# Kernel optimization log

Hardware: AMD Instinct MI355X
Metric: run time of the kernel (lower is better)

The kernel has to match this reference:

```python
import jax, jax.numpy as jnp
import numpy as np
from jax.scipy.optimize import minimize

LAMDA = 0.01        # lamda default in MI()
N_DOMAINS = 2       # domain_label is binary (source/target)
MAXITER = 50        # BFGS iteration budget (torchmin l-bfgs analogue)


def _sq_dists(A, B):
    # squared euclidean pairwise distances == torch.cdist(A, B, p=2) ** 2
    an = jnp.sum(A * A, axis=-1)
    bn = jnp.sum(B * B, axis=-1)
    return an[:, None] + bn[None, :] - 2.0 * (A @ B.T)


def _median_sigma(sf):
    # sigma = median of nonzero squared pairwise source distances.
    # With continuous features the only zeros are the diagonal, so mask it.
    pd = jnp.maximum(_sq_dists(sf, sf), 0.0)
    pd = jnp.where(jnp.eye(pd.shape[0], dtype=bool), jnp.nan, pd)
    return jnp.nanmedian(pd)


def _build(sf, tf, y, l):
    # Gaussian kernel masked by class agreement, plus domain one-hots.
    sigma = _median_sigma(sf)
    X = jnp.concatenate([sf, tf], axis=0)              # [N, d]
    D = _sq_dists(X, X)                                 # [N, N]
    Deltay = (y[:, None] == y[None, :]).astype(X.dtype)
    K_W = jnp.exp(-D / sigma) * Deltay                  # [N, N]
    onehot = jax.nn.one_hot(l[:, 0], N_DOMAINS, dtype=X.dtype)  # [N, 2]
    KD = K_W * (onehot @ onehot.T)                      # K_W * Deltal
    w = jnp.sum(onehot, axis=0) / X.shape[0]            # domain counts / N
    return K_W, KD, onehot, w


def _div(theta, K_W, KD, onehot, w):
    # mean((K_W*Deltal) @ theta) - mean(exp((theta*K_W) @ Deltal - 1))
    # Deltal = onehot @ onehot.T (rank-2), so the second NxN @ NxN matmul
    # collapses to A = K_W @ (theta[:,None]*onehot) with column weights w.
    term1 = jnp.mean(KD @ theta)
    A = K_W @ (theta[:, None] * onehot)                 # [N, 2]
    term2 = jnp.mean(jnp.exp(A - 1.0) @ w)
    return term1 - term2


def _solve_theta(K_W, KD, onehot, w):
    N = K_W.shape[0]
    obj = lambda th: -_div(th, K_W, KD, onehot, w) + LAMDA * (th @ th)
    res = minimize(obj, jnp.zeros((N,), K_W.dtype), method="BFGS",
                   options={"maxiter": MAXITER})
    return res.x


def setup_inputs() -> dict:
    key = jax.random.key(0)
    k1, k2, k3, k4 = jax.random.split(key, 4)
    B, d, n_class = 2048, 256, 31
    source_features = jax.random.normal(k1, (B, d), dtype=jnp.float32)
    target_features = jax.random.normal(k2, (B, d), dtype=jnp.float32)
    y = jax.random.randint(k3, (2 * B,), 0, n_class, dtype=jnp.int32)
    l = jax.random.randint(k4, (2 * B, 1), 0, N_DOMAINS, dtype=jnp.int32)
    return {"source_features": source_features, "target_features": target_features,
            "y": y, "l": l}


def reference(source_features, target_features, y, l):
    K_W, KD, onehot, w = _build(source_features, target_features, y, l)
    theta_hat = _solve_theta(K_W, KD, onehot, w)
    return _div(theta_hat, K_W, KD, onehot, w)
```

## Files before the change

kernel.cpp:

```cpp
#include <hip/hip_runtime.h>
#include <math.h>

#define N_TOT   4096
#define N_SRC   2048
#define DIMF    256
#define NCLASS  31
#define LAMBDA  0.01f

#define K_TRI1  1048063LL
#define K_TRI2  1048064LL

#define WS_ACC    0
#define WS_HIST0  64
#define WS_HISTA  16448
#define WS_HISTB  32832
#define WS_H2A    49216
#define WS_H2B    50240
#define WS_STATE  51264
#define WS_TICK   51520
#define WS_META   52288
#define WS_SCAL   52800
#define ZERO_BYTES 53248
#define WS_PERM   53248
#define WS_XN     69632
#define WS_DS     1048576
#define WS_KBLK   17825792

#define MAXW 224
#define MAXM 112
#define WPAD 116

__device__ __forceinline__ float bf2f(unsigned short h) {
  return __uint_as_float(((unsigned)h) << 16);
}

__device__ __forceinline__ float wredF(float v) {
#pragma unroll
  for (int o = 1; o < 64; o <<= 1) v += __shfl_xor(v, o, 64);
  return v;
}

__device__ __forceinline__ double blockReduceSum(double v, double* red) {
#pragma unroll
  for (int o = 32; o > 0; o >>= 1) v += __shfl_down(v, o, 64);
  int w = threadIdx.x >> 6, lane = threadIdx.x & 63;
  __syncthreads();
  if (lane == 0) red[w] = v;
  __syncthreads();
  return red[0] + red[1] + red[2] + red[3];
}

__device__ __forceinline__ void blockReduceSumMax(double s, double mx, double* red,
                                                  double& os, double& om) {
#pragma unroll
  for (int o = 32; o > 0; o >>= 1) {
    s += __shfl_down(s, o, 64);
    double u = __shfl_down(mx, o, 64);
    mx = fmax(mx, u);
  }
  int w = threadIdx.x >> 6, lane = threadIdx.x & 63;
  __syncthreads();
  if (lane == 0) { red[w] = s; red[4 + w] = mx; }
  __syncthreads();
  os = red[0] + red[1] + red[2] + red[3];
  om = fmax(fmax(red[4], red[5]), fmax(red[6], red[7]));
}

__device__ void scan_find(const unsigned* hist, int nbins, long long k, unsigned* shOut) {
  __shared__ long long tsum[256];
  int tid = threadIdx.x;
  int per = nbins / 256;
  long long s = 0;
  for (int q = 0; q < per; q++) s += hist[tid * per + q];
  tsum[tid] = s;
  __syncthreads();
  long long acc = s;
  for (int off = 1; off < 256; off <<= 1) {
    long long add = (tid >= off) ? tsum[tid - off] : 0;
    __syncthreads();
    acc += add;
    tsum[tid] = acc;
    __syncthreads();
  }
  long long run = acc - s;
  for (int q = 0; q < per; q++) {
    unsigned c = hist[tid * per + q];
    if (k >= run && k < run + (long long)c) { shOut[0] = (unsigned)(tid * per + q); shOut[1] = (unsigned)(k - run); }
    run += c;
  }
  __syncthreads();
}

__global__ __launch_bounds__(256) void xn_kernel(const float* __restrict__ sf,
                                                 const float* __restrict__ tf,
                                                 float* __restrict__ xn) {
  int wid = threadIdx.x >> 6, lane = threadIdx.x & 63;
  int row = blockIdx.x * 4 + wid;
  const float* src = (row < N_SRC) ? (sf + (size_t)row * DIMF) : (tf + (size_t)(row - N_SRC) * DIMF);
  float4 v = ((const float4*)src)[lane];
  float s = v.x * v.x + v.y * v.y + v.z * v.z + v.w * v.w;
#pragma unroll
  for (int o = 32; o > 0; o >>= 1) s += __shfl_down(s, o, 64);
  if (lane == 0) xn[row] = s;
}

__global__ __launch_bounds__(256) void dist_k(const float* __restrict__ sf,
                                              const float* __restrict__ xn,
                                              float* __restrict__ Ds,
                                              unsigned* __restrict__ h) {
  __shared__ float As[16][68];
  __shared__ float Bs[16][68];
  __shared__ unsigned lh[4096];
  const int tx = threadIdx.x, ty = threadIdx.y;
  const int tid = ty * 16 + tx;
  for (int q = tid; q < 4096; q += 256) lh[q] = 0;
  int b = blockIdx.x;
  int by = (int)((sqrtf(8.f * (float)b + 1.f) - 1.f) * 0.5f);
  while ((by + 1) * (by + 2) / 2 <= b) ++by;
  while (by * (by + 1) / 2 > b) --by;
  int bx = b - by * (by + 1) / 2;
  const int R = by * 64, C = bx * 64;
  const int si = tid >> 2, sq = tid & 3;
  float4 va = ((const float4*)(sf + (size_t)(R + si) * 256 + 0))[sq];
  float4 vb = ((const float4*)(sf + (size_t)(C + si) * 256 + 0))[sq];
  float acc[4][4] = {};
  for (int kc = 0; kc < 256; kc += 16) {
    As[sq * 4 + 0][si] = va.x; As[sq * 4 + 1][si] = va.y; As[sq * 4 + 2][si] = va.z; As[sq * 4 + 3][si] = va.w;
    Bs[sq * 4 + 0][si] = vb.x; Bs[sq * 4 + 1][si] = vb.y; Bs[sq * 4 + 2][si] = vb.z; Bs[sq * 4 + 3][si] = vb.w;
    __syncthreads();
    if (kc + 16 < 256) {
      va = ((const float4*)(sf + (size_t)(R + si) * 256 + kc + 16))[sq];
      vb = ((const float4*)(sf + (size_t)(C + si) * 256 + kc + 16))[sq];
    }
#pragma unroll
    for (int k = 0; k < 16; k++) {
      float4 a = *(const float4*)&As[k][ty * 4];
      float4 b2 = *(const float4*)&Bs[k][tx * 4];
      acc[0][0] += a.x * b2.x; acc[0][1] += a.x * b2.y; acc[0][2] += a.x * b2.z; acc[0][3] += a.x * b2.w;
      acc[1][0] += a.y * b2.x; acc[1][1] += a.y * b2.y; acc[1][2] += a.y * b2.z; acc[1][3] += a.y * b2.w;
      acc[2][0] += a.z * b2.x; acc[2][1] += a.z * b2.y; acc[2][2] += a.z * b2.z; acc[2][3] += a.z * b2.w;
      acc[3][0] += a.w * b2.x; acc[3][1] += a.w * b2.y; acc[3][2] += a.w * b2.z; acc[3][3] += a.w * b2.w;
    }
    __syncthreads();
  }
  int jbase = C + tx * 4;
  float xnj0 = xn[jbase + 0], xnj1 = xn[jbase + 1], xnj2 = xn[jbase + 2], xnj3 = xn[jbase + 3];
#pragma unroll
  for (int r = 0; r < 4; r++) {
    int i = R + ty * 4 + r;
    float xni = xn[i];
    float v[4];
    v[0] = fmaxf(xni + xnj0 - 2.f * acc[r][0], 0.f);
    v[1] = fmaxf(xni + xnj1 - 2.f * acc[r][1], 0.f);
    v[2] = fmaxf(xni + xnj2 - 2.f * acc[r][2], 0.f);
    v[3] = fmaxf(xni + xnj3 - 2.f * acc[r][3], 0.f);
    if (jbase + 3 < i) {
      float4 o; o.x = v[0]; o.y = v[1]; o.z = v[2]; o.w = v[3];
      ((float4*)&Ds[(size_t)i * 2048 + jbase])[0] = o;
      atomicAdd(&lh[__float_as_uint(v[0]) >> 20], 1u);
      atomicAdd(&lh[__float_as_uint(v[1]) >> 20], 1u);
      atomicAdd(&lh[__float_as_uint(v[2]) >> 20], 1u);
      atomicAdd(&lh[__float_as_uint(v[3]) >> 20], 1u);
    } else {
#pragma unroll
      for (int k = 0; k < 4; k++) {
        if (jbase + k < i) {
          Ds[(size_t)i * 2048 + jbase + k] = v[k];
          atomicAdd(&lh[__float_as_uint(v[k]) >> 20], 1u);
        }
      }
    }
  }
  __syncthreads();
  for (int q = tid; q < 4096; q += 256) if (lh[q]) atomicAdd(&h[q], lh[q]);
}

__global__ __launch_bounds__(256) void scan0_k(const unsigned* __restrict__ h, unsigned* __restrict__ st) {
  __shared__ unsigned r0[2];
  __shared__ unsigned r1[2];
  scan_find(h, 4096, K_TRI1, r0);
  scan_find(h, 4096, K_TRI2, r1);
  if (threadIdx.x == 0) { st[0] = r0[0]; st[1] = r0[1]; st[2] = r1[0]; st[3] = r1[1]; }
}

__global__ __launch_bounds__(256) void hist1_k(const float* __restrict__ Ds, const unsigned* __restrict__ st,
                                               unsigned* __restrict__ hA, unsigned* __restrict__ hB) {
  __shared__ unsigned lA[4096];
  __shared__ unsigned lB[4096];
  for (int i = threadIdx.x; i < 4096; i += 256) { lA[i] = 0; lB[i] = 0; }
  __syncthreads();
  unsigned s0 = st[0], s1 = st[2];
  int gw = (blockIdx.x * 256 + threadIdx.x) >> 6;
  int lane = threadIdx.x & 63;
  const float* row = Ds + (size_t)gw * 2048;
  for (int j = lane; j < gw; j += 64) {
    unsigned u = __float_as_uint(row[j]);
    unsigned hi = u >> 20, mid = (u >> 8) & 0xFFFu;
    if (hi == s0) atomicAdd(&lA[mid], 1u);
    if (hi == s1) atomicAdd(&lB[mid], 1u);
  }
  __syncthreads();
  for (int i = threadIdx.x; i < 4096; i += 256) {
    if (lA[i]) atomicAdd(&hA[i], lA[i]);
    if (lB[i]) atomicAdd(&hB[i], lB[i]);
  }
}

__global__ __launch_bounds__(256) void scan1_k(const unsigned* __restrict__ hA, const unsigned* __restrict__ hB,
                                               unsigned* __restrict__ st) {
  __shared__ unsigned r0[2];
  __shared__ unsigned r1[2];
  long long kA = (long long)st[1];
  long long kB = (long long)st[3];
  scan_find(hA, 4096, kA, r0);
  scan_find(hB, 4096, kB, r1);
  if (threadIdx.x == 0) { st[4] = r0[0]; st[5] = r0[1]; st[6] = r1[0]; st[7] = r1[1]; }
}

__global__ __launch_bounds__(256) void hist2_k(const float* __restrict__ Ds, const unsigned* __restrict__ st,
                                               unsigned* __restrict__ hA, unsigned* __restrict__ hB) {
  __shared__ unsigned lA[256];
  __shared__ unsigned lB[256];
  lA[threadIdx.x] = 0; lB[threadIdx.x] = 0;
  __syncthreads();
  unsigned p0 = (st[0] << 12) | st[4];
  unsigned p1 = (st[2] << 12) | st[6];
  int gw = (blockIdx.x * 256 + threadIdx.x) >> 6;
  int lane = threadIdx.x & 63;
  const float* row = Ds + (size_t)gw * 2048;
  for (int j = lane; j < gw; j += 64) {
    unsigned u = __float_as_uint(row[j]);
    unsigned pre = u >> 8;
    if (pre == p0) atomicAdd(&lA[u & 0xFFu], 1u);
    if (pre == p1) atomicAdd(&lB[u & 0xFFu], 1u);
  }
  __syncthreads();
  if (lA[threadIdx.x]) atomicAdd(&hA[threadIdx.x], lA[threadIdx.x]);
  if (lB[threadIdx.x]) atomicAdd(&hB[threadIdx.x], lB[threadIdx.x]);
}

__global__ __launch_bounds__(256) void scan2b_k(const unsigned* __restrict__ hA, const unsigned* __restrict__ hB,
                                                const unsigned* __restrict__ st, float* __restrict__ scal,
                                                const int* __restrict__ y, const int* __restrict__ l,
                                                int* __restrict__ perm, int* __restrict__ meta) {
  int tid = threadIdx.x;
  __shared__ unsigned r0[2];
  __shared__ unsigned r1[2];
  scan_find(hA, 256, (long long)st[5], r0);
  scan_find(hB, 256, (long long)st[7], r1);
  if (tid == 0) {
    unsigned v1 = (st[0] << 20) | (st[4] << 8) | r0[0];
    unsigned v2 = (st[2] << 20) | (st[6] << 8) | r1[0];
    scal[0] = 0.5f * (__uint_as_float(v1) + __uint_as_float(v2));
  }
  __shared__ unsigned cl[64];
  __shared__ unsigned bs2[64];
  __shared__ unsigned cur[64];
  if (tid < 64) cl[tid] = 0;
  __syncthreads();
  for (int i = tid; i < N_TOT; i += 256) atomicAdd(&cl[y[i] * 2 + l[i]], 1u);
  __syncthreads();
  if (tid == 0) {
    unsigned run = 0;
    for (int b2 = 0; b2 < 62; b2++) { bs2[b2] = run; run += cl[b2]; }
    unsigned run2 = 0, cnt0 = 0;
    for (int c = 0; c < NCLASS; c++) {
      int n = (int)(cl[2 * c] + cl[2 * c + 1]);
      meta[c] = n; meta[32 + c] = (int)cl[2 * c]; meta[64 + c] = (int)bs2[2 * c];
      meta[96 + c] = (int)run2; run2 += (unsigned)(n * n);
      cnt0 += cl[2 * c];
    }
    scal[1] = (float)((double)cnt0 / (4096.0 * 4096.0));
    scal[2] = (float)((double)(N_TOT - cnt0) / (4096.0 * 4096.0));
  }
  __syncthreads();
  if (tid < 64) cur[tid] = bs2[tid];
  __syncthreads();
  for (int i = tid; i < N_TOT; i += 256) {
    int b2 = y[i] * 2 + l[i];
    unsigned pos = atomicAdd(&cur[b2], 1u);
    perm[pos] = i;
  }
}

__global__ __launch_bounds__(256) void build_k(const float* __restrict__ sf, const float* __restrict__ tf,
                                               const float* __restrict__ xn, const int* __restrict__ perm,
                                               const int* __restrict__ meta, const float* __restrict__ scal,
                                               float* __restrict__ gK) {
  const int c = blockIdx.z;
  const int n = meta[c];
  const int cs = meta[64 + c];
  const int bo = meta[96 + c];
  const int T = (n + 15) >> 4;
  int b = blockIdx.x;
  if (b >= T * (T + 1) / 2) return;
  int by = (int)((sqrtf(8.f * (float)b + 1.f) - 1.f) * 0.5f);
  while ((by + 1) * (by + 2) / 2 <= b) ++by;
  while (by * (by + 1) / 2 > b) --by;
  int bx = b - by * (by + 1) / 2;
  const int i0 = by * 16, j0 = bx * 16;
  const int tx = threadIdx.x, ty = threadIdx.y;
  __shared__ float As[16][260];
  __shared__ float Bs[16][260];
  __shared__ float ot[16][17];
  __shared__ int ra[16];
  __shared__ int rb[16];
  int tid = ty * 16 + tx;
  if (tid < 16) { int il = i0 + tid; ra[tid] = (il < n) ? perm[cs + il] : -1; }
  else if (tid < 32) { int jl = j0 + tid - 16; rb[tid - 16] = (jl < n) ? perm[cs + jl] : -1; }
  __syncthreads();
  for (int e = tid; e < 1024; e += 256) {
    int r = e >> 6, q = e & 63;
    int g = ra[r];
    if (g >= 0) {
      const float* src = (g < N_SRC) ? (sf + (size_t)g * DIMF) : (tf + (size_t)(g - N_SRC) * DIMF);
      ((float4*)&As[r][q * 4])[0] = ((const float4*)src)[q];
    }
    int g2 = rb[r];
    if (g2 >= 0) {
      const float* src = (g2 < N_SRC) ? (sf + (size_t)g2 * DIMF) : (tf + (size_t)(g2 - N_SRC) * DIMF);
      ((float4*)&Bs[r][q * 4])[0] = ((const float4*)src)[q];
    }
  }
  __syncthreads();
  int il = i0 + ty, jl = j0 + tx;
  float val = 0.f;
  if (il < n && jl < n) {
    float dot = 0.f;
    const float4* a4 = (const float4*)&As[ty][0];
    const float4* b4 = (const float4*)&Bs[tx][0];
#pragma unroll 16
    for (int q = 0; q < 64; q++) {
      float4 a = a4[q], b2 = b4[q];
      dot += a.x * b2.x + a.y * b2.y + a.z * b2.z + a.w * b2.w;
    }
    int gi = ra[ty], gj = rb[tx];
    float d = xn[gi] + xn[gj] - 2.f * dot;
    val = expf(-d / scal[0]);
    gK[(size_t)bo + (size_t)il * n + jl] = val;
  }
  ot[ty][tx] = val;
  __syncthreads();
  if (by != bx) {
    int il2 = j0 + ty, jl2 = i0 + tx;
    if (il2 < n && jl2 < n) gK[(size_t)bo + (size_t)il2 * n + jl2] = ot[tx][ty];
  }
}

__global__ __launch_bounds__(256) void solver_k(const float* __restrict__ gK, const int* __restrict__ meta,
                                                const float* __restrict__ scal, double* __restrict__ acc,
                                                unsigned* __restrict__ tick, float* __restrict__ out) {
  const int c = blockIdx.x >> 1, d = blockIdx.x & 1;
  const int n = meta[c];
  const int m0 = meta[32 + c];
  const int m = d ? (n - m0) : m0;
  const int c0 = d ? m0 : 0;
  const int bo = meta[96 + c];
  const float gamma = scal[1 + d];
  const int tid = threadIdx.x;
  const int wv = tid >> 6, lane = tid & 63;

  __shared__ unsigned short Wl[MAXW * WPAD];
  __shared__ float pS[4 * MAXM];
  __shared__ float pD[4 * MAXM];
  __shared__ float Av[MAXW];
  __shared__ float Sv[MAXW];
  __shared__ float Uv[MAXW];
  __shared__ float Bq[MAXW];
  __shared__ float bc[MAXM];
  __shared__ float gv[MAXM];
  __shared__ float dgv[MAXM];
  __shared__ alignas(16) float th[128];
  __shared__ alignas(16) float pv[128];
  __shared__ alignas(16) float xv[128];
  __shared__ double red[16];
  __shared__ double gds[2];
  __shared__ int cgst[2];

  const float* K = gK + bo;
  const int st = n;
  const int mp2 = (m + 1) & ~1;
  const int mp4 = (m + 3) & ~3;
  const int iw0 = (n * wv) >> 2, iw1 = (n * (wv + 1)) >> 2;

  for (int i = tid >> 2; i < n; i += 64) {
    const float* Kr = K + (size_t)i * st + c0;
    unsigned short* Wr = Wl + i * WPAD;
    for (int j = (tid & 3); j < m; j += 4) {
      unsigned u = __float_as_uint(Kr[j]);
      u += 0x7fffu + ((u >> 16) & 1u);
      Wr[j] = (unsigned short)(u >> 16);
    }
    if ((tid & 3) == 0) for (int j = m; j < mp4; j++) Wr[j] = 0;
  }
  {
    const int r0 = (m * wv) >> 2, r1 = (m * (wv + 1)) >> 2;
    for (int j = lane; j < m; j += 64) {
      const float* Kr = K + (size_t)(c0 + j) * st + c0;
      float s = 0.f;
      for (int r = r0; r < r1; r++) s += Kr[r];
      pS[wv * MAXM + j] = s;
    }
  }
  __syncthreads();
  for (int j = tid; j < 128; j += 256) { th[j] = 0.f; pv[j] = 0.f; xv[j] = 0.f; }
  for (int j = tid; j < m; j += 256)
    bc[j] = (pS[j] + pS[MAXM + j] + pS[2 * MAXM + j] + pS[3 * MAXM + j]) * (1.0f / 4096.0f);
  __syncthreads();

  for (int it = 0; it < 25; it++) {
    double o = 0.0;
    if (it == 0) {
      const float s0c = gamma * expf(-1.f);
      for (int i = tid; i < n; i += 256) { Av[i] = 0.f; Sv[i] = s0c; o += (double)s0c; }
    } else {
      for (int i = tid; i < n; i += 256) {
        const unsigned short* Wr = Wl + i * WPAD;
        float a = 0.f;
#pragma unroll 4
        for (int j = 0; j < mp4; j += 4) {
          unsigned long long u = *(const unsigned long long*)(Wr + j);
          float4 t4 = *(const float4*)(th + j);
          unsigned lo = (unsigned)u, hi = (unsigned)(u >> 32);
          a += __uint_as_float(lo << 16) * t4.x
             + __uint_as_float(lo & 0xffff0000u) * t4.y
             + __uint_as_float(hi << 16) * t4.z
             + __uint_as_float(hi & 0xffff0000u) * t4.w;
        }
        Av[i] = a;
        float si = gamma * expf(fminf(a - 1.f, 30.f));
        Sv[i] = si; o += (double)si;
      }
      for (int j = tid; j < m; j += 256) {
        float t_ = th[j];
        o += (double)(-bc[j] * t_ + LAMBDA * t_ * t_);
      }
    }
    __syncthreads();
    if (it == 0) {
      for (int j = lane; j < m; j += 64) {
        const unsigned short* Wc = Wl + j;
        float s_ = 0.f, ds_ = 0.f;
        int i = iw0;
        for (; i + 3 < iw1; i += 4) {
          float w0 = bf2f(Wc[(i + 0) * WPAD]), w1 = bf2f(Wc[(i + 1) * WPAD]);
          float w2 = bf2f(Wc[(i + 2) * WPAD]), w3 = bf2f(Wc[(i + 3) * WPAD]);
          float a0 = w0 * Sv[i], a1 = w1 * Sv[i + 1], a2 = w2 * Sv[i + 2], a3 = w3 * Sv[i + 3];
          s_ += a0 + a1 + a2 + a3;
          ds_ += a0 * w0 + a1 * w1 + a2 * w2 + a3 * w3;
        }
        for (; i < iw1; i++) { float w = bf2f(Wc[i * WPAD]); float a = w * Sv[i]; s_ += a; ds_ += a * w; }
        pS[wv * MAXM + j] = s_; pD[wv * MAXM + j] = ds_;
      }
    } else {
      for (int j = lane; j < m; j += 64) {
        const unsigned short* Wc = Wl + j;
        float s_ = 0.f;
        int i = iw0;
        for (; i + 3 < iw1; i += 4)
          s_ += bf2f(Wc[(i+0)*WPAD]) * Sv[i]   + bf2f(Wc[(i+1)*WPAD]) * Sv[i+1]
              + bf2f(Wc[(i+2)*WPAD]) * Sv[i+2] + bf2f(Wc[(i+3)*WPAD]) * Sv[i+3];
        for (; i < iw1; i++) s_ += bf2f(Wc[i * WPAD]) * Sv[i];
        pS[wv * MAXM + j] = s_;
      }
    }
    __syncthreads();
    double gm = 0.0;
    for (int j = tid; j < m; j += 256) {
      float s_ = pS[j] + pS[MAXM + j] + pS[2 * MAXM + j] + pS[3 * MAXM + j];
      if (it == 0) {
        float ds_ = pD[j] + pD[MAXM + j] + pD[2 * MAXM + j] + pD[3 * MAXM + j];
        dgv[j] = ds_ + 2.f * LAMBDA;
      }
      float g = s_ - bc[j] + 2.f * LAMBDA * th[j];
      gv[j] = g;
      double ag = fabs((double)g); if (ag > gm) gm = ag;
    }
    double obj, gmax;
    blockReduceSumMax(o, gm, red, obj, gmax);
    if (gmax < 1e-5) break;

    const float tolf = (it == 0) ? 1e-2f : ((it == 1) ? 1e-3f : 1e-4f);
    float p0 = 0.f, p1 = 0.f, r0 = 0.f, r1 = 0.f, z0 = 0.f, z1 = 0.f, x0 = 0.f, x1 = 0.f;
    float dg0 = 1.f, dg1 = 1.f, rzf = 0.f, rz0f = 0.f;
    double gtpacc = 0.0;
    const int j0 = lane, j1 = lane + 64;
    if (wv == 0) {
      if (j0 < m) { dg0 = dgv[j0]; r0 = -gv[j0]; z0 = r0 / dg0; }
      if (j1 < m) { dg1 = dgv[j1]; r1 = -gv[j1]; z1 = r1 / dg1; }
      p0 = z0; p1 = z1;
      rzf = wredF(r0 * z0 + r1 * z1);
      rz0f = rzf;
      pv[j0] = p0; pv[j1] = p1;
      if (lane == 0) cgst[0] = (rzf > 0.f) ? 0 : 1;
    }
    __syncthreads();
    for (int cg = 0; cg < 12; cg++) {
      if (cgst[0]) break;
      for (int i = tid; i < n; i += 256) {
        const unsigned short* Wr = Wl + i * WPAD;
        float a = 0.f;
#pragma unroll 4
        for (int j = 0; j < mp4; j += 4) {
          unsigned long long u = *(const unsigned long long*)(Wr + j);
          float4 t4 = *(const float4*)(pv + j);
          unsigned lo = (unsigned)u, hi = (unsigned)(u >> 32);
          a += __uint_as_float(lo << 16) * t4.x
             + __uint_as_float(lo & 0xffff0000u) * t4.y
             + __uint_as_float(hi << 16) * t4.z
             + __uint_as_float(hi & 0xffff0000u) * t4.w;
        }
        Uv[i] = a * Sv[i];
      }
      __syncthreads();
      for (int j = lane; j < m; j += 64) {
        const unsigned short* Wc = Wl + j;
        float q = 0.f;
        int i = iw0;
        for (; i + 3 < iw1; i += 4)
          q += bf2f(Wc[(i+0)*WPAD]) * Uv[i]   + bf2f(Wc[(i+1)*WPAD]) * Uv[i+1]
             + bf2f(Wc[(i+2)*WPAD]) * Uv[i+2] + bf2f(Wc[(i+3)*WPAD]) * Uv[i+3];
        for (; i < iw1; i++) q += bf2f(Wc[i * WPAD]) * Uv[i];
        pS[wv * MAXM + j] = q;
      }
      __syncthreads();
      if (wv == 0) {
        float q0 = 0.f, q1 = 0.f;
        if (j0 < m) q0 = pS[j0] + pS[MAXM + j0] + pS[2*MAXM + j0] + pS[3*MAXM + j0] + 2.f * LAMBDA * p0;
        if (j1 < m) q1 = pS[j1] + pS[MAXM + j1] + pS[2*MAXM + j1] + pS[3*MAXM + j1] + 2.f * LAMBDA * p1;
        float pq = wredF(p0 * q0 + p1 * q1);
        int stop = 0;
        if (!(pq > 0.f)) stop = 1;
        else {
          float alpha = rzf / pq;
          gtpacc += (double)alpha * (double)rzf;
          x0 += alpha * p0; x1 += alpha * p1;
          r0 -= alpha * q0; r1 -= alpha * q1;
          z0 = r0 / dg0;    z1 = r1 / dg1;
          float rzn = wredF(r0 * z0 + r1 * z1);
          if (rzn < tolf * rz0f || cg == 11) stop = 1;
          else {
            float beta = rzn / rzf;
            p0 = z0 + beta * p0; p1 = z1 + beta * p1;
            pv[j0] = p0; pv[j1] = p1;
            rzf = rzn;
          }
        }
        if (lane == 0) cgst[0] = stop;
      }
      __syncthreads();
    }
    if (wv == 0) {
      xv[j0] = x0; xv[j1] = x1;
      if (lane == 0) gds[0] = -gtpacc;
    }
    __syncthreads();
    double gtp = gds[0];
    if (!(gtp < 0.0)) break;

    float t = 1.f;
    if (-gtp >= 1e-4) {
      for (int i = tid; i < n; i += 256) {
        const unsigned short* Wr = Wl + i * WPAD;
        float a = 0.f;
#pragma unroll 4
        for (int j = 0; j < mp4; j += 4) {
          unsigned long long u = *(const unsigned long long*)(Wr + j);
          float4 t4 = *(const float4*)(xv + j);
          unsigned lo = (unsigned)u, hi = (unsigned)(u >> 32);
          a += __uint_as_float(lo << 16) * t4.x
             + __uint_as_float(lo & 0xffff0000u) * t4.y
             + __uint_as_float(hi << 16) * t4.z
             + __uint_as_float(hi & 0xffff0000u) * t4.w;
        }
        Bq[i] = a;
      }
      __syncthreads();
      for (int ls = 0; ls < 10; ls++) {
        double ol = 0.0;
        for (int i = tid; i < n; i += 256)
          ol += (double)(gamma * expf(fminf(Av[i] + t * Bq[i] - 1.f, 30.f)));
        for (int j = tid; j < m; j += 256) {
          float tj = th[j] + t * xv[j];
          ol += (double)(-bc[j] * tj + LAMBDA * tj * tj);
        }
        double ot2 = blockReduceSum(ol, red);
        if (ot2 <= obj + 1e-4 * (double)t * gtp) break;
        t *= 0.5f;
      }
    }
    for (int j = tid; j < mp2; j += 256) th[j] += t * xv[j];
    __syncthreads();
  }

  __syncthreads();
  for (int i = tid; i < n; i += 256) {
    const float* Kr = K + (size_t)i * st + c0;
    float a = 0.f;
    int j = 0;
    for (; j + 7 < m; j += 8)
      a += th[j] * Kr[j] + th[j+1] * Kr[j+1] + th[j+2] * Kr[j+2] + th[j+3] * Kr[j+3]
         + th[j+4] * Kr[j+4] + th[j+5] * Kr[j+5] + th[j+6] * Kr[j+6] + th[j+7] * Kr[j+7];
    for (; j < m; j++) a += th[j] * Kr[j];
    Av[i] = a;
  }
  __syncthreads();
  double t1l = 0.0, t2l = 0.0;
  for (int i = tid; i < n; i += 256) t2l += (double)(gamma * expf(fminf(Av[i] - 1.f, 30.f)));
  for (int j = tid; j < m; j += 256) t1l += (double)(bc[j] * th[j]);
  double t1 = blockReduceSum(t1l, red);
  double t2 = blockReduceSum(t2l, red);
  if (tid == 0) {
    atomicAdd(&acc[0], t1);
    atomicAdd(&acc[1], t2);
    __threadfence();
    unsigned old = __hip_atomic_fetch_add(&tick[0], 1u, __ATOMIC_ACQ_REL, __HIP_MEMORY_SCOPE_AGENT);
    if (old == 61u) {
      double a0 = __hip_atomic_load(&acc[0], __ATOMIC_RELAXED, __HIP_MEMORY_SCOPE_AGENT);
      double a1 = __hip_atomic_load(&acc[1], __ATOMIC_RELAXED, __HIP_MEMORY_SCOPE_AGENT);
      out[0] = (float)(a0 - a1);
    }
  }
}

extern "C" void kernel_launch(void* const* d_in, const int* in_sizes, int n_in,
                              void* d_out, int out_size, void* d_ws, size_t ws_size,
                              hipStream_t stream) {
  const float* sf = (const float*)d_in[0];
  const float* tf = (const float*)d_in[1];
  const int* y = (const int*)d_in[2];
  const int* l = (const int*)d_in[3];
  char* ws = (char*)d_ws;

  double*   acc    = (double*)(ws + WS_ACC);
  unsigned* hist0  = (unsigned*)(ws + WS_HIST0);
  unsigned* histA  = (unsigned*)(ws + WS_HISTA);
  unsigned* histB  = (unsigned*)(ws + WS_HISTB);
  unsigned* h2A    = (unsigned*)(ws + WS_H2A);
  unsigned* h2B    = (unsigned*)(ws + WS_H2B);
  unsigned* state  = (unsigned*)(ws + WS_STATE);
  unsigned* tick   = (unsigned*)(ws + WS_TICK);
  int*      meta   = (int*)(ws + WS_META);
  float*    scal   = (float*)(ws + WS_SCAL);
  int*      perm   = (int*)(ws + WS_PERM);
  float*    xnp    = (float*)(ws + WS_XN);
  float*    Ds     = (float*)(ws + WS_DS);
  float*    gK     = (float*)(ws + WS_KBLK);

  hipMemsetAsync(d_ws, 0, ZERO_BYTES, stream);
  hipLaunchKernelGGL(xn_kernel, dim3(1024), dim3(256), 0, stream, sf, tf, xnp);
  hipLaunchKernelGGL(dist_k, dim3(528), dim3(16, 16), 0, stream, sf, xnp, Ds, hist0);
  hipLaunchKernelGGL(scan0_k, dim3(1), dim3(256), 0, stream, hist0, state);
  hipLaunchKernelGGL(hist1_k, dim3(512), dim3(256), 0, stream, Ds, state, histA, histB);
  hipLaunchKernelGGL(scan1_k, dim3(1), dim3(256), 0, stream, histA, histB, state);
  hipLaunchKernelGGL(hist2_k, dim3(512), dim3(256), 0, stream, Ds, state, h2A, h2B);
  hipLaunchKernelGGL(scan2b_k, dim3(1), dim3(256), 0, stream, h2A, h2B, state, scal, y, l, perm, meta);
  hipLaunchKernelGGL(build_k, dim3(105, 1, NCLASS), dim3(16, 16), 0, stream, sf, tf, xnp, perm, meta, scal, gK);
  hipLaunchKernelGGL(solver_k, dim3(62), dim3(256), 0, stream, gK, meta, scal, acc, tick, (float*)d_out);
}
```

Baseline: 209.3 us.

## Fold workspace memset into xn kernel, split LDS histogram, lane-parallel solver rows

The workspace zeroing moves from a separate hipMemsetAsync into block 0 of xn_kernel, which removes one stream operation. The distance kernel keeps two shared histograms selected by thread parity to reduce LDS atomic contention, then merges them before the global atomics. In the solver, the bias column sums and the final K·theta products now give each row to four lanes and combine them with shuffles, which makes global reads more parallel and drops the pS scratch reduction. These are several independent micro-optimizations. The memset fold relies on dist_k's atomics to hist0 being ordered after xn_kernel on the same stream.

```diff
diff --git a/kernel.cpp b/kernel.cpp
--- a/kernel.cpp
+++ b/kernel.cpp
@@ -66,9 +66,8 @@
   om = fmax(fmax(red[4], red[5]), fmax(red[6], red[7]));
 }
 
-__device__ void scan_find(const unsigned* hist, int nbins, long long k, unsigned* shOut) {
+__device__ void scan_find(const unsigned* hist, int nbins, long long k, unsigned* shOut, int tid) {
   __shared__ long long tsum[256];
-  int tid = threadIdx.x;
   int per = nbins / 256;
   long long s = 0;
   for (int q = 0; q < per; q++) s += hist[tid * per + q];
@@ -93,7 +92,12 @@
 
 __global__ __launch_bounds__(256) void xn_kernel(const float* __restrict__ sf,
                                                  const float* __restrict__ tf,
-                                                 float* __restrict__ xn) {
+                                                 float* __restrict__ xn,
+                                                 uint4* __restrict__ wsz) {
+  if (blockIdx.x == 0) {
+    uint4 z; z.x = 0; z.y = 0; z.z = 0; z.w = 0;
+    for (int q = threadIdx.x; q < ZERO_BYTES / 16; q += 256) wsz[q] = z;
+  }
   int wid = threadIdx.x >> 6, lane = threadIdx.x & 63;
   int row = blockIdx.x * 4 + wid;
   const float* src = (row < N_SRC) ? (sf + (size_t)row * DIMF) : (tf + (size_t)(row - N_SRC) * DIMF);
@@ -110,10 +114,11 @@
                                               unsigned* __restrict__ h) {
   __shared__ float As[16][68];
   __shared__ float Bs[16][68];
-  __shared__ unsigned lh[4096];
+  __shared__ unsigned lh[2][4096];
   const int tx = threadIdx.x, ty = threadIdx.y;
   const int tid = ty * 16 + tx;
-  for (int q = tid; q < 4096; q += 256) lh[q] = 0;
+  const int par = tid & 1;
+  for (int q = tid; q < 8192; q += 256) lh[q >> 12][q & 4095] = 0;
   int b = blockIdx.x;
   int by = (int)((sqrtf(8.f * (float)b + 1.f) - 1.f) * 0.5f);
   while ((by + 1) * (by + 2) / 2 <= b) ++by;
@@ -157,29 +162,32 @@
     if (jbase + 3 < i) {
       float4 o; o.x = v[0]; o.y = v[1]; o.z = v[2]; o.w = v[3];
       ((float4*)&Ds[(size_t)i * 2048 + jbase])[0] = o;
-      atomicAdd(&lh[__float_as_uint(v[0]) >> 20], 1u);
-      atomicAdd(&lh[__float_as_uint(v[1]) >> 20], 1u);
-      atomicAdd(&lh[__float_as_uint(v[2]) >> 20], 1u);
-      atomicAdd(&lh[__float_as_uint(v[3]) >> 20], 1u);
+      atomicAdd(&lh[par][__float_as_uint(v[0]) >> 20], 1u);
+      atomicAdd(&lh[par][__float_as_uint(v[1]) >> 20], 1u);
+      atomicAdd(&lh[par][__float_as_uint(v[2]) >> 20], 1u);
+      atomicAdd(&lh[par][__float_as_uint(v[3]) >> 20], 1u);
     } else {
 #pragma unroll
       for (int k = 0; k < 4; k++) {
         if (jbase + k < i) {
           Ds[(size_t)i * 2048 + jbase + k] = v[k];
-          atomicAdd(&lh[__float_as_uint(v[k]) >> 20], 1u);
+          atomicAdd(&lh[par][__float_as_uint(v[k]) >> 20], 1u);
         }
       }
     }
   }
   __syncthreads();
-  for (int q = tid; q < 4096; q += 256) if (lh[q]) atomicAdd(&h[q], lh[q]);
+  for (int q = tid; q < 4096; q += 256) {
+    unsigned v = lh[0][q] + lh[1][q];
+    if (v) atomicAdd(&h[q], v);
+  }
 }
 
 __global__ __launch_bounds__(256) void scan0_k(const unsigned* __restrict__ h, unsigned* __restrict__ st) {
   __shared__ unsigned r0[2];
   __shared__ unsigned r1[2];
-  scan_find(h, 4096, K_TRI1, r0);
-  scan_find(h, 4096, K_TRI2, r1);
+  scan_find(h, 4096, K_TRI1, r0, threadIdx.x);
+  scan_find(h, 4096, K_TRI2, r1, threadIdx.x);
   if (threadIdx.x == 0) { st[0] = r0[0]; st[1] = r0[1]; st[2] = r1[0]; st[3] = r1[1]; }
 }
 
@@ -212,8 +220,8 @@
   __shared__ unsigned r1[2];
   long long kA = (long long)st[1];
   long long kB = (long long)st[3];
-  scan_find(hA, 4096, kA, r0);
-  scan_find(hB, 4096, kB, r1);
+  scan_find(hA, 4096, kA, r0, threadIdx.x);
+  scan_find(hB, 4096, kB, r1, threadIdx.x);
   if (threadIdx.x == 0) { st[4] = r0[0]; st[5] = r0[1]; st[6] = r1[0]; st[7] = r1[1]; }
 }
 
@@ -246,8 +254,8 @@
   int tid = threadIdx.x;
   __shared__ unsigned r0[2];
   __shared__ unsigned r1[2];
-  scan_find(hA, 256, (long long)st[5], r0);
-  scan_find(hB, 256, (long long)st[7], r1);
+  scan_find(hA, 256, (long long)st[5], r0, tid);
+  scan_find(hB, 256, (long long)st[7], r1, tid);
   if (tid == 0) {
     unsigned v1 = (st[0] << 20) | (st[4] << 8) | r0[0];
     unsigned v2 = (st[2] << 20) | (st[6] << 8) | r1[0];
@@ -382,30 +390,28 @@
   const int mp2 = (m + 1) & ~1;
   const int mp4 = (m + 3) & ~3;
   const int iw0 = (n * wv) >> 2, iw1 = (n * (wv + 1)) >> 2;
-
-  for (int i = tid >> 2; i < n; i += 64) {
+  const int rq = tid >> 2, ql = tid & 3;
+
+  for (int i = rq; i < n; i += 64) {
     const float* Kr = K + (size_t)i * st + c0;
     unsigned short* Wr = Wl + i * WPAD;
-    for (int j = (tid & 3); j < m; j += 4) {
+    for (int j = ql; j < m; j += 4) {
       unsigned u = __float_as_uint(Kr[j]);
       u += 0x7fffu + ((u >> 16) & 1u);
       Wr[j] = (unsigned short)(u >> 16);
     }
-    if ((tid & 3) == 0) for (int j = m; j < mp4; j++) Wr[j] = 0;
-  }
-  {
-    const int r0 = (m * wv) >> 2, r1 = (m * (wv + 1)) >> 2;
-    for (int j = lane; j < m; j += 64) {
-      const float* Kr = K + (size_t)(c0 + j) * st + c0;
-      float s = 0.f;
-      for (int r = r0; r < r1; r++) s += Kr[r];
-      pS[wv * MAXM + j] = s;
-    }
+    if (ql == 0) for (int j = m; j < mp4; j++) Wr[j] = 0;
+  }
+  for (int j = rq; j < m; j += 64) {
+    const float* Kr = K + (size_t)(c0 + j) * st + c0;
+    float s = 0.f;
+    for (int r = ql; r < m; r += 4) s += Kr[r];
+    s += __shfl_xor(s, 1, 64);
+    s += __shfl_xor(s, 2, 64);
+    if (ql == 0) bc[j] = s * (1.0f / 4096.0f);
   }
   __syncthreads();
   for (int j = tid; j < 128; j += 256) { th[j] = 0.f; pv[j] = 0.f; xv[j] = 0.f; }
-  for (int j = tid; j < m; j += 256)
-    bc[j] = (pS[j] + pS[MAXM + j] + pS[2 * MAXM + j] + pS[3 * MAXM + j]) * (1.0f / 4096.0f);
   __syncthreads();
 
   for (int it = 0; it < 25; it++) {
@@ -594,15 +600,14 @@
   }
 
   __syncthreads();
-  for (int i = tid; i < n; i += 256) {
+  for (int i = rq; i < n; i += 64) {
     const float* Kr = K + (size_t)i * st + c0;
     float a = 0.f;
-    int j = 0;
-    for (; j + 7 < m; j += 8)
-      a += th[j] * Kr[j] + th[j+1] * Kr[j+1] + th[j+2] * Kr[j+2] + th[j+3] * Kr[j+3]
-         + th[j+4] * Kr[j+4] + th[j+5] * Kr[j+5] + th[j+6] * Kr[j+6] + th[j+7] * Kr[j+7];
-    for (; j < m; j++) a += th[j] * Kr[j];
-    Av[i] = a;
+#pragma unroll 4
+    for (int j = ql; j < m; j += 4) a += th[j] * Kr[j];
+    a += __shfl_xor(a, 1, 64);
+    a += __shfl_xor(a, 2, 64);
+    if (ql == 0) Av[i] = a;
   }
   __syncthreads();
   double t1l = 0.0, t2l = 0.0;
@@ -647,8 +652,7 @@
   float*    Ds     = (float*)(ws + WS_DS);
   float*    gK     = (float*)(ws + WS_KBLK);
 
-  hipMemsetAsync(d_ws, 0, ZERO_BYTES, stream);
-  hipLaunchKernelGGL(xn_kernel, dim3(1024), dim3(256), 0, stream, sf, tf, xnp);
+  hipLaunchKernelGGL(xn_kernel, dim3(1024), dim3(256), 0, stream, sf, tf, xnp, (uint4*)ws);
   hipLaunchKernelGGL(dist_k, dim3(528), dim3(16, 16), 0, stream, sf, xnp, Ds, hist0);
   hipLaunchKernelGGL(scan0_k, dim3(1), dim3(256), 0, stream, hist0, state);
   hipLaunchKernelGGL(hist1_k, dim3(512), dim3(256), 0, stream, Ds, state, histA, histB);
```

Result: no change. 206.9 us (-1.1%).
